# Kernel tuning notes

Measured on AMD Instinct MI355X. Metric: run time of the kernel, lower is better.

## Reference

```python
import jax, jax.numpy as jnp
import numpy as np

B, H, D = 4096, 1024, 4
SCALE = 20.0
EPS = 1e-7
LABEL_GATE = 0.01


def _layer_norm(x, g, b, eps=1e-5):
    mu = jnp.mean(x, axis=-1, keepdims=True)
    var = jnp.mean(jnp.square(x - mu), axis=-1, keepdims=True)
    return (x - mu) * jax.lax.rsqrt(var + eps) * g + b


def setup_inputs() -> dict:
    key = jax.random.key(0)
    ks = jax.random.split(key, 8)
    s = 0.02
    return {
        "pooled": jax.random.normal(ks[0], (B, H), dtype=jnp.float32),
        "labels": jax.random.uniform(ks[1], (B, D), dtype=jnp.float32),
        "ln1_g": jnp.ones((H,), jnp.float32),
        "ln1_b": jnp.zeros((H,), jnp.float32),
        "W1": jax.random.normal(ks[2], (H, H // 2), dtype=jnp.float32) * s,
        "b1": jnp.zeros((H // 2,), jnp.float32),
        "ln2_g": jnp.ones((H // 2,), jnp.float32),
        "ln2_b": jnp.zeros((H // 2,), jnp.float32),
        "W2": jax.random.normal(ks[3], (H // 2, H // 4), dtype=jnp.float32) * s,
        "b2": jnp.zeros((H // 4,), jnp.float32),
        "Wh": jax.random.normal(ks[4], (H // 4, D), dtype=jnp.float32) * s,
        "bh": jnp.zeros((D,), jnp.float32),
    }


def reference(pooled, labels, ln1_g, ln1_b, W1, b1, ln2_g, ln2_b, W2, b2, Wh, bh):
    # MLP head (dropout = identity in eval mode); exact GELU as in torch nn.GELU
    h1 = jax.nn.gelu(_layer_norm(pooled, ln1_g, ln1_b) @ W1 + b1, approximate=False)
    h2 = jax.nn.gelu(_layer_norm(h1, ln2_g, ln2_b) @ W2 + b2, approximate=False)
    logits = jax.nn.sigmoid(h2 @ Wh + bh)  # [B, D]

    # MSE term
    mse = jnp.mean(jnp.square(logits - labels))

    # Vectorized pairwise ordering loss over all i<j pairs and dims
    ldiff = labels[:, None, :] - labels[None, :, :]   # [B, B, D]
    pdiff = logits[:, None, :] - logits[None, :, :]   # [B, B, D]
    target_prob = jax.nn.sigmoid(SCALE * ldiff)
    pred_prob = jax.nn.sigmoid(SCALE * pdiff)
    bce = -target_prob * jnp.log(pred_prob + EPS) - (1.0 - target_prob) * jnp.log(1.0 - pred_prob + EPS)

    iu = jnp.triu(jnp.ones((B, B), dtype=bool), k=1)[:, :, None]  # i < j
    mask = iu & (jnp.abs(ldiff) > LABEL_GATE)
    cnt = jnp.sum(mask)
    ordering = jnp.where(cnt > 0, jnp.sum(jnp.where(mask, bce, 0.0)) / jnp.maximum(cnt, 1).astype(bce.dtype), 0.0)

    loss = 0.5 * mse + 0.5 * ordering
    return loss, logits
```

## Files before the change

### kernel.cpp

```cpp
#include <hip/hip_runtime.h>
#include <math.h>
#include <stdint.h>

typedef unsigned short u16;
typedef unsigned long long u64;
typedef __attribute__((ext_vector_type(8))) short bf16x8;
typedef __attribute__((ext_vector_type(4))) float f32x4;

#define RSQRT1_2F 0.70710678118654752440f

__device__ __forceinline__ u16 rne_bf16(float x) {
  unsigned u = __float_as_uint(x);
  return (u16)((u + 0x7FFFu + ((u >> 16) & 1u)) >> 16);
}
__device__ __forceinline__ float bf16_to_f(u16 h) {
  return __uint_as_float(((unsigned)h) << 16);
}
__device__ __forceinline__ void gload_lds16(const void* g, void* l) {
  __builtin_amdgcn_global_load_lds(
      (__attribute__((address_space(1))) void*)(uintptr_t)g,
      (__attribute__((address_space(3))) void*)(uintptr_t)l, 16, 0, 0);
}
__device__ __forceinline__ float rlane(float v, int sl) {
  return __uint_as_float((unsigned)__builtin_amdgcn_readlane((int)__float_as_uint(v), sl));
}
__device__ __forceinline__ float block_reduce_sum_f(float v, float* smem4) {
  #pragma unroll
  for (int off = 32; off > 0; off >>= 1) v += __shfl_down(v, off, 64);
  const int lane = threadIdx.x & 63;
  const int wid  = threadIdx.x >> 6;
  if (lane == 0) smem4[wid] = v;
  __syncthreads();
  float r = smem4[0] + smem4[1] + smem4[2] + smem4[3];
  __syncthreads();
  return r;
}
__device__ __forceinline__ float gelu_exact(float z) {
  return 0.5f * z * (1.0f + erff(z * RSQRT1_2F));
}

template<int H, int NPT>
__device__ __forceinline__ void ln_split_body(
    const float* __restrict__ x, const float* __restrict__ g,
    const float* __restrict__ b, u16* __restrict__ yhi, u16* __restrict__ ylo,
    int row, float* smem4) {
  const float* xr = x + (size_t)row * H;
  const int tid = threadIdx.x;
  float v[NPT];
  #pragma unroll
  for (int q = 0; q < NPT; ++q) v[q] = xr[tid + q * 256];
  float s = 0.f;
  #pragma unroll
  for (int q = 0; q < NPT; ++q) s += v[q];
  s = block_reduce_sum_f(s, smem4);
  const float mu = s * (1.0f / H);
  float s2 = 0.f;
  #pragma unroll
  for (int q = 0; q < NPT; ++q) { float d = v[q] - mu; s2 = fmaf(d, d, s2); }
  s2 = block_reduce_sum_f(s2, smem4);
  const float rstd = rsqrtf(s2 * (1.0f / H) + 1e-5f);
  #pragma unroll
  for (int q = 0; q < NPT; ++q) {
    const int c = tid + q * 256;
    const float y = (v[q] - mu) * rstd * g[c] + b[c];
    const u16 h = rne_bf16(y);
    const u16 lo = rne_bf16(y - bf16_to_f(h));
    yhi[(size_t)row * H + c] = h;
    ylo[(size_t)row * H + c] = lo;
  }
}

template<int K, int N>
__device__ __forceinline__ void wsplit_body(
    const float* __restrict__ W, u16* __restrict__ Whi, u16* __restrict__ Wlo,
    int ntile, int ktile, float* sm ) {
  const int t = threadIdx.x;
  const int n0 = ntile * 64, k0 = ktile * 64;
  #pragma unroll
  for (int q = 0; q < 16; ++q) {
    const int r = q * 4 + (t >> 6);
    sm[r * 65 + (t & 63)] = W[(size_t)(k0 + r) * N + n0 + (t & 63)];
  }
  __syncthreads();
  #pragma unroll
  for (int q = 0; q < 16; ++q) {
    const int nr = q * 4 + (t >> 6);
    const int kc = t & 63;
    const float v = sm[kc * 65 + nr];
    const u16 h = rne_bf16(v);
    const u16 lo = rne_bf16(v - bf16_to_f(h));
    Whi[(size_t)(n0 + nr) * K + k0 + kc] = h;
    Wlo[(size_t)(n0 + nr) * K + k0 + kc] = lo;
  }
}

__global__ __launch_bounds__(256) void prep_kernel(
    const float* __restrict__ pooled, const float* __restrict__ ln1_g,
    const float* __restrict__ ln1_b, const float* __restrict__ W1,
    const float* __restrict__ W2,
    u16* __restrict__ xhi, u16* __restrict__ xlo,
    u16* __restrict__ w1thi, u16* __restrict__ w1tlo,
    u16* __restrict__ w2thi, u16* __restrict__ w2tlo) {
  __shared__ float sm[64 * 65];
  const int bid = blockIdx.x;
  if (bid < 4096) {
    ln_split_body<1024, 4>(pooled, ln1_g, ln1_b, xhi, xlo, bid, sm);
  } else if (bid < 4224) {
    const int idx = bid - 4096;
    wsplit_body<1024, 512>(W1, w1thi, w1tlo, idx & 7, idx >> 3, sm);
  } else {
    const int idx = bid - 4224;
    wsplit_body<512, 256>(W2, w2thi, w2tlo, idx & 3, idx >> 2, sm);
  }
}

template<int H, int NPT>
__global__ __launch_bounds__(256) void ln_gelu_split_kernel(
    const float* __restrict__ Pa, const float* __restrict__ Pb,
    const float* __restrict__ bias, const float* __restrict__ g,
    const float* __restrict__ b, u16* __restrict__ yhi, u16* __restrict__ ylo) {
  __shared__ float smem4[4];
  const int row = blockIdx.x;
  const size_t base = (size_t)row * H;
  const int tid = threadIdx.x;
  float v[NPT];
  #pragma unroll
  for (int q = 0; q < NPT; ++q) {
    const int c = tid + q * 256;
    v[q] = gelu_exact(Pa[base + c] + Pb[base + c] + bias[c]);
  }
  float s = 0.f;
  #pragma unroll
  for (int q = 0; q < NPT; ++q) s += v[q];
  s = block_reduce_sum_f(s, smem4);
  const float mu = s * (1.0f / H);
  float s2 = 0.f;
  #pragma unroll
  for (int q = 0; q < NPT; ++q) { float d = v[q] - mu; s2 = fmaf(d, d, s2); }
  s2 = block_reduce_sum_f(s2, smem4);
  const float rstd = rsqrtf(s2 * (1.0f / H) + 1e-5f);
  #pragma unroll
  for (int q = 0; q < NPT; ++q) {
    const int c = tid + q * 256;
    const float y = (v[q] - mu) * rstd * g[c] + b[c];
    const u16 h = rne_bf16(y);
    const u16 lo = rne_bf16(y - bf16_to_f(h));
    yhi[base + c] = h;
    ylo[base + c] = lo;
  }
}

template<int M, int N, int K, int KCH>
__global__ __launch_bounds__(256, 2) void gemm_bf16x3_partial(
    const u16* __restrict__ Ahi, const u16* __restrict__ Alo,
    const u16* __restrict__ Bhi, const u16* __restrict__ Blo,
    float* __restrict__ P, double* zclr) {
  if (zclr && blockIdx.x == 0 && blockIdx.y == 0 && blockIdx.z == 0 &&
      threadIdx.x < 32) {
    zclr[threadIdx.x] = 0.0;
    zclr[32 + threadIdx.x] = 0.0;
    ((u64*)(zclr + 64))[threadIdx.x] = 0ull;
  }
  __shared__ __align__(16) char sb[49152];
  const int t = threadIdx.x;
  const int w = t >> 6;
  const int l = t & 63;
  const int lm = l & 15, lk = l >> 4;
  const int wm = w >> 1, wn = w & 1;

  const int gx = gridDim.x, gy = gridDim.y;
  const int nwg = gx * gy * gridDim.z;
  const int bid = blockIdx.x + gx * (blockIdx.y + gy * blockIdx.z);
  int swz = (bid & 7) * (nwg >> 3) + (bid >> 3);
  const int bx = swz % gx; swz /= gx;
  const int by = swz % gy;
  const int bz = swz / gy;

  const int m0 = by * 128, n0 = bx * 64;
  const int kbase = bz * KCH;
  float* __restrict__ Pz = P + (size_t)bz * M * N;

  f32x4 acc[4][2];
  #pragma unroll
  for (int m = 0; m < 4; ++m)
    #pragma unroll
    for (int n = 0; n < 2; ++n)
      #pragma unroll
      for (int r = 0; r < 4; ++r) acc[m][n][r] = 0.f;

  const int srow = t >> 3;
  const int sslot = (t & 7) * 16;

  for (int k0 = kbase; k0 < kbase + KCH; k0 += 64) {
    #pragma unroll
    for (int q = 0; q < 4; ++q) {
      const int row = q * 32 + srow;
      const int cl = sslot ^ ((row & 7) << 4);
      const size_t gb = ((size_t)(m0 + row) * K + k0) * 2 + cl;
      gload_lds16((const char*)Ahi + gb, sb + q * 4096 + w * 1024);
      gload_lds16((const char*)Alo + gb, sb + 16384 + q * 4096 + w * 1024);
    }
    #pragma unroll
    for (int q = 0; q < 2; ++q) {
      const int row = q * 32 + srow;
      const int cl = sslot ^ ((row & 7) << 4);
      const size_t gb = ((size_t)(n0 + row) * K + k0) * 2 + cl;
      gload_lds16((const char*)Bhi + gb, sb + 32768 + q * 4096 + w * 1024);
      gload_lds16((const char*)Blo + gb, sb + 40960 + q * 4096 + w * 1024);
    }
    __syncthreads();

    #pragma unroll
    for (int kk = 0; kk < 2; ++kk) {
      const int cbase = kk * 64 + lk * 16;
      bf16x8 ah[4], al[4];
      #pragma unroll
      for (int m = 0; m < 4; ++m) {
        const int row = wm * 64 + m * 16 + lm;
        const int c = cbase ^ ((row & 7) << 4);
        ah[m] = *(const bf16x8*)(sb + row * 128 + c);
        al[m] = *(const bf16x8*)(sb + 16384 + row * 128 + c);
      }
      bf16x8 bh[2], bl[2];
      #pragma unroll
      for (int n = 0; n < 2; ++n) {
        const int row = wn * 32 + n * 16 + lm;
        const int c = cbase ^ ((row & 7) << 4);
        bh[n] = *(const bf16x8*)(sb + 32768 + row * 128 + c);
        bl[n] = *(const bf16x8*)(sb + 40960 + row * 128 + c);
      }
      #pragma unroll
      for (int m = 0; m < 4; ++m)
        #pragma unroll
        for (int n = 0; n < 2; ++n) {
          acc[m][n] = __builtin_amdgcn_mfma_f32_16x16x32_bf16(ah[m], bh[n], acc[m][n], 0, 0, 0);
          acc[m][n] = __builtin_amdgcn_mfma_f32_16x16x32_bf16(ah[m], bl[n], acc[m][n], 0, 0, 0);
          acc[m][n] = __builtin_amdgcn_mfma_f32_16x16x32_bf16(al[m], bh[n], acc[m][n], 0, 0, 0);
        }
    }
    __syncthreads();
  }

  #pragma unroll
  for (int m = 0; m < 4; ++m)
    #pragma unroll
    for (int n = 0; n < 2; ++n) {
      const int col = n0 + wn * 32 + n * 16 + lm;
      #pragma unroll
      for (int r = 0; r < 4; ++r) {
        const int row = m0 + wm * 64 + m * 16 + lk * 4 + r;
        Pz[(size_t)row * N + col] = acc[m][n][r];
      }
    }
}

template<int NZ>
__global__ __launch_bounds__(256) void head_kernel(
    const float* __restrict__ P2, const float* __restrict__ b2,
    const float* __restrict__ Wh, const float* __restrict__ bh,
    const float* __restrict__ labels,
    float* __restrict__ logits_out, float* __restrict__ To,
    float* __restrict__ Eo, float* __restrict__ Lo,
    double* __restrict__ mse_slots) {
  const int lane = threadIdx.x & 63;
  const int wv   = threadIdx.x >> 6;
  const int row  = blockIdx.x * 4 + wv;
  const size_t base = (size_t)row * 256;
  constexpr size_t ZSTRIDE = (size_t)4096 * 256;
  float a0 = 0.f, a1 = 0.f, a2 = 0.f, a3 = 0.f;
  #pragma unroll
  for (int q = 0; q < 4; ++q) {
    const int k = lane + q * 64;
    float s = b2[k];
    #pragma unroll
    for (int z = 0; z < NZ; ++z) s += P2[z * ZSTRIDE + base + k];
    const float hv = gelu_exact(s);
    const float4 wv4 = *(const float4*)&Wh[k * 4];
    a0 = fmaf(hv, wv4.x, a0); a1 = fmaf(hv, wv4.y, a1);
    a2 = fmaf(hv, wv4.z, a2); a3 = fmaf(hv, wv4.w, a3);
  }
  #pragma unroll
  for (int off = 32; off > 0; off >>= 1) {
    a0 += __shfl_down(a0, off, 64);
    a1 += __shfl_down(a1, off, 64);
    a2 += __shfl_down(a2, off, 64);
    a3 += __shfl_down(a3, off, 64);
  }
  if (lane == 0) {
    const float z[4] = {a0 + bh[0], a1 + bh[1], a2 + bh[2], a3 + bh[3]};
    float msew = 0.f;
    #pragma unroll
    for (int d = 0; d < 4; ++d) {
      const float p = 1.0f / (1.0f + expf(-z[d]));
      const float lab = labels[row * 4 + d];
      logits_out[row * 4 + d] = p;
      To[row * 4 + d] = 20.0f * p;
      Eo[row * 4 + d] = expf(20.0f * p);
      Lo[row * 4 + d] = expf(20.0f * lab);
      const float df = p - lab;
      msew = fmaf(df, df, msew);
    }
    atomicAdd(&mse_slots[row & 31], (double)msew);
  }
}

#define GFUN(t) ((t) * 64 - (t) * ((t) - 1) / 2)
#define TGATE 0.0498339962f

__global__ __launch_bounds__(256) void pairwise_kernel(
    const float* __restrict__ To, const float* __restrict__ E,
    const float* __restrict__ L, double* __restrict__ slots) {
  const int lane = threadIdx.x & 63;
  const int wv   = threadIdx.x >> 6;
  const int idx  = blockIdx.x * 4 + wv;
  const int tile = idx >> 1;
  const int jbase = (idx & 1) * 32;

  int ti = (int)((129.0f - sqrtf(fmaxf(16641.0f - 8.0f * (float)tile, 0.f))) * 0.5f);
  if (ti < 0) ti = 0; if (ti > 63) ti = 63;
  while (ti > 0 && GFUN(ti) > tile) ti--;
  while (ti < 63 && GFUN(ti + 1) <= tile) ti++;
  const int tj = ti + (tile - GFUN(ti));
  const int i0 = ti * 64, j0 = tj * 64;
  const int i = i0 + lane, j = j0 + lane;

  const float4 e4 = *(const float4*)&E[(size_t)i * 4];
  const float4 t4 = *(const float4*)&To[(size_t)i * 4];
  const float4 l4 = *(const float4*)&L[(size_t)i * 4];
  const float Ei[4] = {e4.x, e4.y, e4.z, e4.w};
  const float Ti[4] = {t4.x, t4.y, t4.z, t4.w};
  const float Li[4] = {l4.x, l4.y, l4.z, l4.w};
  const float4 ej4 = *(const float4*)&E[(size_t)j * 4];
  const float4 tj4 = *(const float4*)&To[(size_t)j * 4];
  const float4 lj4 = *(const float4*)&L[(size_t)j * 4];
  const float Ejv[4] = {ej4.x, ej4.y, ej4.z, ej4.w};
  const float Tjv[4] = {tj4.x, tj4.y, tj4.z, tj4.w};
  const float Ljv[4] = {lj4.x, lj4.y, lj4.z, lj4.w};

  const bool diag = (ti == tj);
  float acc[4] = {0.f, 0.f, 0.f, 0.f};
  int cnt = 0;
  #pragma unroll 8
  for (int s = 0; s < 32; ++s) {
    const int jj = jbase + s;
    const bool jok = !diag || (jj > lane);
    #pragma unroll
    for (int d = 0; d < 4; ++d) {
      const float Ej = rlane(Ejv[d], jj);
      const float Tj = rlane(Tjv[d], jj);
      const float Lj = rlane(Ljv[d], jj);
      const float logse = __logf(Ei[d] + Ej);
      const float tt = Li[d] * __builtin_amdgcn_rcpf(Li[d] + Lj);
      const float bce = (logse - Tj) - tt * (Ti[d] - Tj);
      const bool m = jok && (fabsf(tt - 0.5f) > TGATE);
      acc[d] += m ? bce : 0.f;
      cnt += m ? 1 : 0;
    }
  }

  float tot = (acc[0] + acc[1]) + (acc[2] + acc[3]);
  #pragma unroll
  for (int off = 32; off > 0; off >>= 1) {
    tot += __shfl_down(tot, off, 64);
    cnt += __shfl_down(cnt, off, 64);
  }
  if (lane == 0) {
    const int sl = idx & 31;
    atomicAdd(&slots[32 + sl], (double)tot);
    atomicAdd((u64*)(slots + 64) + sl, (u64)cnt);
  }
}

__global__ void finalize_kernel(const double* __restrict__ slots,
                                float* __restrict__ out) {
  const int l = threadIdx.x;
  double m = (l < 32) ? slots[l] : 0.0;
  double o = (l < 32) ? slots[32 + l] : 0.0;
  double c = (l < 32) ? (double)((const u64*)(slots + 64))[l] : 0.0;
  #pragma unroll
  for (int off = 32; off > 0; off >>= 1) {
    m += __shfl_down(m, off, 64);
    o += __shfl_down(o, off, 64);
    c += __shfl_down(c, off, 64);
  }
  if (l == 0) {
    const double mse = m / (4096.0 * 4.0);
    const double ord = (c > 0.0) ? (o / c) : 0.0;
    out[0] = (float)(0.5 * mse + 0.5 * ord);
  }
}

extern "C" void kernel_launch(void* const* d_in, const int* in_sizes, int n_in,
                              void* d_out, int out_size, void* d_ws, size_t ws_size,
                              hipStream_t stream) {
  const float* pooled = (const float*)d_in[0];
  const float* labels = (const float*)d_in[1];
  const float* ln1_g  = (const float*)d_in[2];
  const float* ln1_b  = (const float*)d_in[3];
  const float* W1     = (const float*)d_in[4];
  const float* b1     = (const float*)d_in[5];
  const float* ln2_g  = (const float*)d_in[6];
  const float* ln2_b  = (const float*)d_in[7];
  const float* W2     = (const float*)d_in[8];
  const float* b2     = (const float*)d_in[9];
  const float* Wh     = (const float*)d_in[10];
  const float* bh     = (const float*)d_in[11];
  float* out = (float*)d_out;

  char* ws = (char*)d_ws;
  u16*   xhi   = (u16*)(ws + 0);
  u16*   xlo   = (u16*)(ws + 8388608);
  u16*   w1thi = (u16*)(ws + 16777216);
  u16*   w1tlo = (u16*)(ws + 17825792);
  float* P1    = (float*)(ws + 18874368);
  u16*   h1nhi = (u16*)(ws + 0);
  u16*   h1nlo = (u16*)(ws + 4194304);
  u16*   w2thi = (u16*)(ws + 8388608);
  u16*   w2tlo = (u16*)(ws + 8650752);
  float* P2    = (float*)(ws + 8912896);
  float* Eo    = (float*)(ws + 25690112);
  float* To    = (float*)(ws + 25755648);
  float* Lo    = (float*)(ws + 25821184);
  double* slots = (double*)(ws + 25886720);

  prep_kernel<<<4256, 256, 0, stream>>>(pooled, ln1_g, ln1_b, W1, W2,
                                        xhi, xlo, w1thi, w1tlo, w2thi, w2tlo);
  gemm_bf16x3_partial<4096, 512, 1024, 512><<<dim3(8, 32, 2), 256, 0, stream>>>(
      xhi, xlo, w1thi, w1tlo, P1, nullptr);
  ln_gelu_split_kernel<512, 2><<<4096, 256, 0, stream>>>(
      P1, P1 + (size_t)4096 * 512, b1, ln2_g, ln2_b, h1nhi, h1nlo);
  gemm_bf16x3_partial<4096, 256, 512, 128><<<dim3(4, 32, 4), 256, 0, stream>>>(
      h1nhi, h1nlo, w2thi, w2tlo, P2, slots);
  head_kernel<4><<<1024, 256, 0, stream>>>(
      P2, b2, Wh, bh, labels, out + 1, To, Eo, Lo, slots);
  pairwise_kernel<<<1040, 256, 0, stream>>>(To, Eo, Lo, slots);
  finalize_kernel<<<1, 64, 0, stream>>>(slots, out);
}
```

Baseline: 190.3 us.

## Fuse all stages into one persistent kernel with software grid barriers

Replaces the seven-kernel launch chain with a single persistent 512-block kernel that runs prep, both GEMMs, LN/GELU, head, pairwise loss and finalize as phases separated by a two-level atomic grid barrier. The aim is to remove kernel launch gaps and tail effects between the small stages. Row-wise LayerNorm moves to one wave per row with shuffle-only reductions, and the GEMM now uses a double-buffered BK=32 LDS pipeline. The cost is spin-wait barriers that assume all 512 blocks are co-resident, a bounded spin that could silently break, and a fixed grid that may underuse the device in some phases.

```diff
diff --git a/kernel.cpp b/kernel.cpp
--- a/kernel.cpp
+++ b/kernel.cpp
@@ -8,6 +8,8 @@
 typedef __attribute__((ext_vector_type(4))) float f32x4;
 
 #define RSQRT1_2F 0.70710678118654752440f
+#define MB 1048576UL
+#define NBLK 512
 
 __device__ __forceinline__ u16 rne_bf16(float x) {
   unsigned u = __float_as_uint(x);
@@ -24,50 +26,36 @@
 __device__ __forceinline__ float rlane(float v, int sl) {
   return __uint_as_float((unsigned)__builtin_amdgcn_readlane((int)__float_as_uint(v), sl));
 }
-__device__ __forceinline__ float block_reduce_sum_f(float v, float* smem4) {
+__device__ __forceinline__ float wave_sum(float v) {
   #pragma unroll
-  for (int off = 32; off > 0; off >>= 1) v += __shfl_down(v, off, 64);
-  const int lane = threadIdx.x & 63;
-  const int wid  = threadIdx.x >> 6;
-  if (lane == 0) smem4[wid] = v;
-  __syncthreads();
-  float r = smem4[0] + smem4[1] + smem4[2] + smem4[3];
-  __syncthreads();
-  return r;
+  for (int off = 32; off > 0; off >>= 1) v += __shfl_xor(v, off, 64);
+  return v;
 }
 __device__ __forceinline__ float gelu_exact(float z) {
   return 0.5f * z * (1.0f + erff(z * RSQRT1_2F));
 }
 
-template<int H, int NPT>
-__device__ __forceinline__ void ln_split_body(
-    const float* __restrict__ x, const float* __restrict__ g,
-    const float* __restrict__ b, u16* __restrict__ yhi, u16* __restrict__ ylo,
-    int row, float* smem4) {
-  const float* xr = x + (size_t)row * H;
-  const int tid = threadIdx.x;
-  float v[NPT];
-  #pragma unroll
-  for (int q = 0; q < NPT; ++q) v[q] = xr[tid + q * 256];
-  float s = 0.f;
-  #pragma unroll
-  for (int q = 0; q < NPT; ++q) s += v[q];
-  s = block_reduce_sum_f(s, smem4);
-  const float mu = s * (1.0f / H);
-  float s2 = 0.f;
-  #pragma unroll
-  for (int q = 0; q < NPT; ++q) { float d = v[q] - mu; s2 = fmaf(d, d, s2); }
-  s2 = block_reduce_sum_f(s2, smem4);
-  const float rstd = rsqrtf(s2 * (1.0f / H) + 1e-5f);
-  #pragma unroll
-  for (int q = 0; q < NPT; ++q) {
-    const int c = tid + q * 256;
-    const float y = (v[q] - mu) * rstd * g[c] + b[c];
-    const u16 h = rne_bf16(y);
-    const u16 lo = rne_bf16(y - bf16_to_f(h));
-    yhi[(size_t)row * H + c] = h;
-    ylo[(size_t)row * H + c] = lo;
-  }
+__device__ __forceinline__ void grid_sync(char* bar, int phase) {
+  __syncthreads();
+  if (threadIdx.x == 0) {
+    unsigned* L1   = (unsigned*)(bar + phase * 4096);
+    unsigned* L2   = (unsigned*)(bar + phase * 4096 + 2048);
+    unsigned* flag = (unsigned*)(bar + phase * 4096 + 2176);
+    __threadfence();
+    if (atomicAdd(&L1[(blockIdx.x & 31) * 16], 1u) == 15u) {
+      if (atomicAdd(L2, 1u) == 31u) {
+        __threadfence();
+        atomicExch(flag, 1u);
+      }
+    }
+    int iters = 0;
+    while (__hip_atomic_load(flag, __ATOMIC_RELAXED, __HIP_MEMORY_SCOPE_AGENT) == 0u) {
+      __builtin_amdgcn_s_sleep(2);
+      if (++iters > (1 << 22)) break;
+    }
+    __threadfence();
+  }
+  __syncthreads();
 }
 
 template<int K, int N>
@@ -92,93 +80,27 @@
     Whi[(size_t)(n0 + nr) * K + k0 + kc] = h;
     Wlo[(size_t)(n0 + nr) * K + k0 + kc] = lo;
   }
-}
-
-__global__ __launch_bounds__(256) void prep_kernel(
-    const float* __restrict__ pooled, const float* __restrict__ ln1_g,
-    const float* __restrict__ ln1_b, const float* __restrict__ W1,
-    const float* __restrict__ W2,
-    u16* __restrict__ xhi, u16* __restrict__ xlo,
-    u16* __restrict__ w1thi, u16* __restrict__ w1tlo,
-    u16* __restrict__ w2thi, u16* __restrict__ w2tlo) {
-  __shared__ float sm[64 * 65];
-  const int bid = blockIdx.x;
-  if (bid < 4096) {
-    ln_split_body<1024, 4>(pooled, ln1_g, ln1_b, xhi, xlo, bid, sm);
-  } else if (bid < 4224) {
-    const int idx = bid - 4096;
-    wsplit_body<1024, 512>(W1, w1thi, w1tlo, idx & 7, idx >> 3, sm);
-  } else {
-    const int idx = bid - 4224;
-    wsplit_body<512, 256>(W2, w2thi, w2tlo, idx & 3, idx >> 2, sm);
-  }
-}
-
-template<int H, int NPT>
-__global__ __launch_bounds__(256) void ln_gelu_split_kernel(
-    const float* __restrict__ Pa, const float* __restrict__ Pb,
-    const float* __restrict__ bias, const float* __restrict__ g,
-    const float* __restrict__ b, u16* __restrict__ yhi, u16* __restrict__ ylo) {
-  __shared__ float smem4[4];
-  const int row = blockIdx.x;
-  const size_t base = (size_t)row * H;
-  const int tid = threadIdx.x;
-  float v[NPT];
-  #pragma unroll
-  for (int q = 0; q < NPT; ++q) {
-    const int c = tid + q * 256;
-    v[q] = gelu_exact(Pa[base + c] + Pb[base + c] + bias[c]);
-  }
-  float s = 0.f;
-  #pragma unroll
-  for (int q = 0; q < NPT; ++q) s += v[q];
-  s = block_reduce_sum_f(s, smem4);
-  const float mu = s * (1.0f / H);
-  float s2 = 0.f;
-  #pragma unroll
-  for (int q = 0; q < NPT; ++q) { float d = v[q] - mu; s2 = fmaf(d, d, s2); }
-  s2 = block_reduce_sum_f(s2, smem4);
-  const float rstd = rsqrtf(s2 * (1.0f / H) + 1e-5f);
-  #pragma unroll
-  for (int q = 0; q < NPT; ++q) {
-    const int c = tid + q * 256;
-    const float y = (v[q] - mu) * rstd * g[c] + b[c];
-    const u16 h = rne_bf16(y);
-    const u16 lo = rne_bf16(y - bf16_to_f(h));
-    yhi[base + c] = h;
-    ylo[base + c] = lo;
-  }
-}
-
-template<int M, int N, int K, int KCH>
-__global__ __launch_bounds__(256, 2) void gemm_bf16x3_partial(
-    const u16* __restrict__ Ahi, const u16* __restrict__ Alo,
-    const u16* __restrict__ Bhi, const u16* __restrict__ Blo,
-    float* __restrict__ P, double* zclr) {
-  if (zclr && blockIdx.x == 0 && blockIdx.y == 0 && blockIdx.z == 0 &&
-      threadIdx.x < 32) {
-    zclr[threadIdx.x] = 0.0;
-    zclr[32 + threadIdx.x] = 0.0;
-    ((u64*)(zclr + 64))[threadIdx.x] = 0ull;
-  }
-  __shared__ __align__(16) char sb[49152];
-  const int t = threadIdx.x;
-  const int w = t >> 6;
-  const int l = t & 63;
-  const int lm = l & 15, lk = l >> 4;
+  __syncthreads();
+}
+
+template<int NX, int MY, int NZ, int K>
+__device__ void gemm_phase(const u16* __restrict__ Ahi, const u16* __restrict__ Alo,
+                           const u16* __restrict__ Bhi, const u16* __restrict__ Blo,
+                           float* __restrict__ P, char* sb) {
+  constexpr int BN = 64, M = 4096;
+  constexpr int N = BN * NX;
+  constexpr int KCH = K / NZ;
+  constexpr int NS = KCH / 32;
+  constexpr int BUF = 24576;
+  const int t = threadIdx.x, w = t >> 6, l = t & 63, lm = l & 15, lk = l >> 4;
   const int wm = w >> 1, wn = w & 1;
-
-  const int gx = gridDim.x, gy = gridDim.y;
-  const int nwg = gx * gy * gridDim.z;
-  const int bid = blockIdx.x + gx * (blockIdx.y + gy * blockIdx.z);
-  int swz = (bid & 7) * (nwg >> 3) + (bid >> 3);
-  const int bx = swz % gx; swz /= gx;
-  const int by = swz % gy;
-  const int bz = swz / gy;
-
-  const int m0 = by * 128, n0 = bx * 64;
-  const int kbase = bz * KCH;
-  float* __restrict__ Pz = P + (size_t)bz * M * N;
+  int bid = (int)blockIdx.x;
+  bid = (bid & 7) * 64 + (bid >> 3);
+  const int z = bid / (NX * MY);
+  const int rem = bid % (NX * MY);
+  const int my = rem / NX, nx = rem % NX;
+  const int m0 = my * 128, n0 = nx * BN, kbase = z * KCH;
+  float* __restrict__ Pz = P + (size_t)z * M * N;
 
   f32x4 acc[4][2];
   #pragma unroll
@@ -188,56 +110,59 @@
       #pragma unroll
       for (int r = 0; r < 4; ++r) acc[m][n][r] = 0.f;
 
-  const int srow = t >> 3;
-  const int sslot = (t & 7) * 16;
-
-  for (int k0 = kbase; k0 < kbase + KCH; k0 += 64) {
-    #pragma unroll
-    for (int q = 0; q < 4; ++q) {
-      const int row = q * 32 + srow;
-      const int cl = sslot ^ ((row & 7) << 4);
-      const size_t gb = ((size_t)(m0 + row) * K + k0) * 2 + cl;
-      gload_lds16((const char*)Ahi + gb, sb + q * 4096 + w * 1024);
-      gload_lds16((const char*)Alo + gb, sb + 16384 + q * 4096 + w * 1024);
-    }
+  const int trow = t >> 2;
+  const int tcol = (t & 3) * 16;
+
+  auto STAGE = [&](int bufsel, int k0) {
+    char* bb = sb + bufsel * BUF;
     #pragma unroll
     for (int q = 0; q < 2; ++q) {
-      const int row = q * 32 + srow;
-      const int cl = sslot ^ ((row & 7) << 4);
-      const size_t gb = ((size_t)(n0 + row) * K + k0) * 2 + cl;
-      gload_lds16((const char*)Bhi + gb, sb + 32768 + q * 4096 + w * 1024);
-      gload_lds16((const char*)Blo + gb, sb + 40960 + q * 4096 + w * 1024);
-    }
-    __syncthreads();
-
-    #pragma unroll
-    for (int kk = 0; kk < 2; ++kk) {
-      const int cbase = kk * 64 + lk * 16;
-      bf16x8 ah[4], al[4];
-      #pragma unroll
-      for (int m = 0; m < 4; ++m) {
-        const int row = wm * 64 + m * 16 + lm;
-        const int c = cbase ^ ((row & 7) << 4);
-        ah[m] = *(const bf16x8*)(sb + row * 128 + c);
-        al[m] = *(const bf16x8*)(sb + 16384 + row * 128 + c);
-      }
-      bf16x8 bh[2], bl[2];
+      const int row = q * 64 + trow;
+      const int col = tcol ^ (((row >> 1) & 3) << 4);
+      const size_t gb = ((size_t)(m0 + row) * K + k0) * 2 + col;
+      gload_lds16((const char*)Ahi + gb, bb + q * 4096 + t * 16);
+      gload_lds16((const char*)Alo + gb, bb + 8192 + q * 4096 + t * 16);
+    }
+    {
+      const int row = trow;
+      const int col = tcol ^ (((row >> 1) & 3) << 4);
+      const size_t gb = ((size_t)(n0 + row) * K + k0) * 2 + col;
+      gload_lds16((const char*)Bhi + gb, bb + 16384 + t * 16);
+      gload_lds16((const char*)Blo + gb, bb + 20480 + t * 16);
+    }
+  };
+  auto COMPUTE = [&](int bufsel) {
+    char* bb = sb + bufsel * BUF;
+    bf16x8 ah[4], al[4], bhv[2], blv[2];
+    #pragma unroll
+    for (int m = 0; m < 4; ++m) {
+      const int row = wm * 64 + m * 16 + lm;
+      const int col = (lk * 16) ^ (((row >> 1) & 3) << 4);
+      ah[m] = *(const bf16x8*)(bb + row * 64 + col);
+      al[m] = *(const bf16x8*)(bb + 8192 + row * 64 + col);
+    }
+    #pragma unroll
+    for (int n = 0; n < 2; ++n) {
+      const int row = wn * 32 + n * 16 + lm;
+      const int col = (lk * 16) ^ (((row >> 1) & 3) << 4);
+      bhv[n] = *(const bf16x8*)(bb + 16384 + row * 64 + col);
+      blv[n] = *(const bf16x8*)(bb + 20480 + row * 64 + col);
+    }
+    #pragma unroll
+    for (int m = 0; m < 4; ++m)
       #pragma unroll
       for (int n = 0; n < 2; ++n) {
-        const int row = wn * 32 + n * 16 + lm;
-        const int c = cbase ^ ((row & 7) << 4);
-        bh[n] = *(const bf16x8*)(sb + 32768 + row * 128 + c);
-        bl[n] = *(const bf16x8*)(sb + 40960 + row * 128 + c);
-      }
-      #pragma unroll
-      for (int m = 0; m < 4; ++m)
-        #pragma unroll
-        for (int n = 0; n < 2; ++n) {
-          acc[m][n] = __builtin_amdgcn_mfma_f32_16x16x32_bf16(ah[m], bh[n], acc[m][n], 0, 0, 0);
-          acc[m][n] = __builtin_amdgcn_mfma_f32_16x16x32_bf16(ah[m], bl[n], acc[m][n], 0, 0, 0);
-          acc[m][n] = __builtin_amdgcn_mfma_f32_16x16x32_bf16(al[m], bh[n], acc[m][n], 0, 0, 0);
-        }
-    }
+        acc[m][n] = __builtin_amdgcn_mfma_f32_16x16x32_bf16(ah[m], bhv[n], acc[m][n], 0, 0, 0);
+        acc[m][n] = __builtin_amdgcn_mfma_f32_16x16x32_bf16(ah[m], blv[n], acc[m][n], 0, 0, 0);
+        acc[m][n] = __builtin_amdgcn_mfma_f32_16x16x32_bf16(al[m], bhv[n], acc[m][n], 0, 0, 0);
+      }
+  };
+
+  STAGE(0, kbase);
+  __syncthreads();
+  for (int s = 0; s < NS; ++s) {
+    if (s + 1 < NS) STAGE((s + 1) & 1, kbase + (s + 1) * 32);
+    COMPUTE(s & 1);
     __syncthreads();
   }
 
@@ -254,139 +179,239 @@
     }
 }
 
-template<int NZ>
-__global__ __launch_bounds__(256) void head_kernel(
-    const float* __restrict__ P2, const float* __restrict__ b2,
-    const float* __restrict__ Wh, const float* __restrict__ bh,
-    const float* __restrict__ labels,
-    float* __restrict__ logits_out, float* __restrict__ To,
-    float* __restrict__ Eo, float* __restrict__ Lo,
-    double* __restrict__ mse_slots) {
-  const int lane = threadIdx.x & 63;
-  const int wv   = threadIdx.x >> 6;
-  const int row  = blockIdx.x * 4 + wv;
-  const size_t base = (size_t)row * 256;
-  constexpr size_t ZSTRIDE = (size_t)4096 * 256;
-  float a0 = 0.f, a1 = 0.f, a2 = 0.f, a3 = 0.f;
-  #pragma unroll
-  for (int q = 0; q < 4; ++q) {
-    const int k = lane + q * 64;
-    float s = b2[k];
-    #pragma unroll
-    for (int z = 0; z < NZ; ++z) s += P2[z * ZSTRIDE + base + k];
-    const float hv = gelu_exact(s);
-    const float4 wv4 = *(const float4*)&Wh[k * 4];
-    a0 = fmaf(hv, wv4.x, a0); a1 = fmaf(hv, wv4.y, a1);
-    a2 = fmaf(hv, wv4.z, a2); a3 = fmaf(hv, wv4.w, a3);
-  }
-  #pragma unroll
-  for (int off = 32; off > 0; off >>= 1) {
-    a0 += __shfl_down(a0, off, 64);
-    a1 += __shfl_down(a1, off, 64);
-    a2 += __shfl_down(a2, off, 64);
-    a3 += __shfl_down(a3, off, 64);
-  }
-  if (lane == 0) {
-    const float z[4] = {a0 + bh[0], a1 + bh[1], a2 + bh[2], a3 + bh[3]};
-    float msew = 0.f;
-    #pragma unroll
-    for (int d = 0; d < 4; ++d) {
-      const float p = 1.0f / (1.0f + expf(-z[d]));
-      const float lab = labels[row * 4 + d];
-      logits_out[row * 4 + d] = p;
-      To[row * 4 + d] = 20.0f * p;
-      Eo[row * 4 + d] = expf(20.0f * p);
-      Lo[row * 4 + d] = expf(20.0f * lab);
-      const float df = p - lab;
-      msew = fmaf(df, df, msew);
-    }
-    atomicAdd(&mse_slots[row & 31], (double)msew);
-  }
-}
-
 #define GFUN(t) ((t) * 64 - (t) * ((t) - 1) / 2)
 #define TGATE 0.0498339962f
 
-__global__ __launch_bounds__(256) void pairwise_kernel(
-    const float* __restrict__ To, const float* __restrict__ E,
-    const float* __restrict__ L, double* __restrict__ slots) {
-  const int lane = threadIdx.x & 63;
-  const int wv   = threadIdx.x >> 6;
-  const int idx  = blockIdx.x * 4 + wv;
-  const int tile = idx >> 1;
-  const int jbase = (idx & 1) * 32;
-
-  int ti = (int)((129.0f - sqrtf(fmaxf(16641.0f - 8.0f * (float)tile, 0.f))) * 0.5f);
-  if (ti < 0) ti = 0; if (ti > 63) ti = 63;
-  while (ti > 0 && GFUN(ti) > tile) ti--;
-  while (ti < 63 && GFUN(ti + 1) <= tile) ti++;
-  const int tj = ti + (tile - GFUN(ti));
-  const int i0 = ti * 64, j0 = tj * 64;
-  const int i = i0 + lane, j = j0 + lane;
-
-  const float4 e4 = *(const float4*)&E[(size_t)i * 4];
-  const float4 t4 = *(const float4*)&To[(size_t)i * 4];
-  const float4 l4 = *(const float4*)&L[(size_t)i * 4];
-  const float Ei[4] = {e4.x, e4.y, e4.z, e4.w};
-  const float Ti[4] = {t4.x, t4.y, t4.z, t4.w};
-  const float Li[4] = {l4.x, l4.y, l4.z, l4.w};
-  const float4 ej4 = *(const float4*)&E[(size_t)j * 4];
-  const float4 tj4 = *(const float4*)&To[(size_t)j * 4];
-  const float4 lj4 = *(const float4*)&L[(size_t)j * 4];
-  const float Ejv[4] = {ej4.x, ej4.y, ej4.z, ej4.w};
-  const float Tjv[4] = {tj4.x, tj4.y, tj4.z, tj4.w};
-  const float Ljv[4] = {lj4.x, lj4.y, lj4.z, lj4.w};
-
-  const bool diag = (ti == tj);
-  float acc[4] = {0.f, 0.f, 0.f, 0.f};
-  int cnt = 0;
-  #pragma unroll 8
-  for (int s = 0; s < 32; ++s) {
-    const int jj = jbase + s;
-    const bool jok = !diag || (jj > lane);
-    #pragma unroll
-    for (int d = 0; d < 4; ++d) {
-      const float Ej = rlane(Ejv[d], jj);
-      const float Tj = rlane(Tjv[d], jj);
-      const float Lj = rlane(Ljv[d], jj);
-      const float logse = __logf(Ei[d] + Ej);
-      const float tt = Li[d] * __builtin_amdgcn_rcpf(Li[d] + Lj);
-      const float bce = (logse - Tj) - tt * (Ti[d] - Tj);
-      const bool m = jok && (fabsf(tt - 0.5f) > TGATE);
-      acc[d] += m ? bce : 0.f;
-      cnt += m ? 1 : 0;
-    }
-  }
-
-  float tot = (acc[0] + acc[1]) + (acc[2] + acc[3]);
-  #pragma unroll
-  for (int off = 32; off > 0; off >>= 1) {
-    tot += __shfl_down(tot, off, 64);
-    cnt += __shfl_down(cnt, off, 64);
-  }
-  if (lane == 0) {
-    const int sl = idx & 31;
-    atomicAdd(&slots[32 + sl], (double)tot);
-    atomicAdd((u64*)(slots + 64) + sl, (u64)cnt);
-  }
-}
-
-__global__ void finalize_kernel(const double* __restrict__ slots,
-                                float* __restrict__ out) {
-  const int l = threadIdx.x;
-  double m = (l < 32) ? slots[l] : 0.0;
-  double o = (l < 32) ? slots[32 + l] : 0.0;
-  double c = (l < 32) ? (double)((const u64*)(slots + 64))[l] : 0.0;
-  #pragma unroll
-  for (int off = 32; off > 0; off >>= 1) {
-    m += __shfl_down(m, off, 64);
-    o += __shfl_down(o, off, 64);
-    c += __shfl_down(c, off, 64);
-  }
-  if (l == 0) {
-    const double mse = m / (4096.0 * 4.0);
-    const double ord = (c > 0.0) ? (o / c) : 0.0;
-    out[0] = (float)(0.5 * mse + 0.5 * ord);
+__global__ __launch_bounds__(256, 2) void mega_kernel(
+    const float* __restrict__ pooled, const float* __restrict__ labels,
+    const float* __restrict__ ln1_g, const float* __restrict__ ln1_b,
+    const float* __restrict__ W1, const float* __restrict__ b1,
+    const float* __restrict__ ln2_g, const float* __restrict__ ln2_b,
+    const float* __restrict__ W2, const float* __restrict__ b2,
+    const float* __restrict__ Wh, const float* __restrict__ bh,
+    float* __restrict__ out, char* __restrict__ ws) {
+  __shared__ __align__(16) char sb[49152];
+
+  u16*   xhi   = (u16*)(ws);
+  u16*   xlo   = (u16*)(ws + 8 * MB);
+  u16*   w1thi = (u16*)(ws + 16 * MB);
+  u16*   w1tlo = (u16*)(ws + 17 * MB);
+  u16*   w2thi = (u16*)(ws + 18 * MB);
+  u16*   w2tlo = (u16*)(ws + 18 * MB + 262144);
+  float* P1    = (float*)(ws + 19 * MB);
+  u16*   h1nhi = (u16*)(ws + 35 * MB);
+  u16*   h1nlo = (u16*)(ws + 39 * MB);
+  float* P2    = (float*)(ws + 43 * MB);
+  float* Eo    = (float*)(ws + 59 * MB);
+  float* To    = (float*)(ws + 59 * MB + 65536);
+  float* Lo    = (float*)(ws + 59 * MB + 131072);
+  char*  bar   = ws + 60 * MB;
+  double* S    = (double*)(ws + 60 * MB + 24576);
+
+  const int t = threadIdx.x, w = t >> 6, l = t & 63;
+  const int bid = (int)blockIdx.x;
+  const int gw = bid * 4 + w;
+
+  {
+    #pragma unroll
+    for (int pass = 0; pass < 2; ++pass) {
+      const int row = gw + pass * 2048;
+      const float* xr = pooled + (size_t)row * 1024;
+      float v[16];
+      #pragma unroll
+      for (int q = 0; q < 16; ++q) v[q] = xr[l + q * 64];
+      float s = 0.f;
+      #pragma unroll
+      for (int q = 0; q < 16; ++q) s += v[q];
+      s = wave_sum(s);
+      const float mu = s * (1.0f / 1024.0f);
+      float s2 = 0.f;
+      #pragma unroll
+      for (int q = 0; q < 16; ++q) { float d = v[q] - mu; s2 = fmaf(d, d, s2); }
+      s2 = wave_sum(s2);
+      const float rstd = rsqrtf(s2 * (1.0f / 1024.0f) + 1e-5f);
+      const size_t base = (size_t)row * 1024;
+      #pragma unroll
+      for (int q = 0; q < 16; ++q) {
+        const int c = l + q * 64;
+        const float y = (v[q] - mu) * rstd * ln1_g[c] + ln1_b[c];
+        const u16 h = rne_bf16(y);
+        xhi[base + c] = h;
+        xlo[base + c] = rne_bf16(y - bf16_to_f(h));
+      }
+    }
+    if (bid < 160) {
+      __syncthreads();
+      float* sm = (float*)sb;
+      if (bid < 128) wsplit_body<1024, 512>(W1, w1thi, w1tlo, bid & 7, bid >> 3, sm);
+      else           wsplit_body<512, 256>(W2, w2thi, w2tlo, (bid - 128) & 3, (bid - 128) >> 2, sm);
+    }
+  }
+  grid_sync(bar, 0);
+
+  gemm_phase<8, 32, 2, 1024>(xhi, xlo, w1thi, w1tlo, P1, sb);
+  grid_sync(bar, 1);
+
+  {
+    constexpr size_t ZS1 = (size_t)4096 * 512;
+    #pragma unroll
+    for (int pass = 0; pass < 2; ++pass) {
+      const int row = gw + pass * 2048;
+      const size_t base = (size_t)row * 512;
+      float v[8];
+      #pragma unroll
+      for (int q = 0; q < 8; ++q) {
+        const int c = l + q * 64;
+        float s = b1[c] + P1[base + c] + P1[ZS1 + base + c];
+        v[q] = gelu_exact(s);
+      }
+      float s = 0.f;
+      #pragma unroll
+      for (int q = 0; q < 8; ++q) s += v[q];
+      s = wave_sum(s);
+      const float mu = s * (1.0f / 512.0f);
+      float s2 = 0.f;
+      #pragma unroll
+      for (int q = 0; q < 8; ++q) { float d = v[q] - mu; s2 = fmaf(d, d, s2); }
+      s2 = wave_sum(s2);
+      const float rstd = rsqrtf(s2 * (1.0f / 512.0f) + 1e-5f);
+      #pragma unroll
+      for (int q = 0; q < 8; ++q) {
+        const int c = l + q * 64;
+        const float y = (v[q] - mu) * rstd * ln2_g[c] + ln2_b[c];
+        const u16 h = rne_bf16(y);
+        h1nhi[base + c] = h;
+        h1nlo[base + c] = rne_bf16(y - bf16_to_f(h));
+      }
+    }
+  }
+  grid_sync(bar, 2);
+
+  gemm_phase<4, 32, 4, 512>(h1nhi, h1nlo, w2thi, w2tlo, P2, sb);
+  grid_sync(bar, 3);
+
+  {
+    constexpr size_t ZS2 = (size_t)4096 * 256;
+    #pragma unroll
+    for (int pass = 0; pass < 2; ++pass) {
+      const int row = gw + pass * 2048;
+      const size_t base = (size_t)row * 256;
+      float a0 = 0.f, a1 = 0.f, a2 = 0.f, a3 = 0.f;
+      #pragma unroll
+      for (int q = 0; q < 4; ++q) {
+        const int k = l + q * 64;
+        float s = b2[k];
+        #pragma unroll
+        for (int z = 0; z < 4; ++z) s += P2[z * ZS2 + base + k];
+        const float hv = gelu_exact(s);
+        const float4 w4 = *(const float4*)&Wh[k * 4];
+        a0 = fmaf(hv, w4.x, a0); a1 = fmaf(hv, w4.y, a1);
+        a2 = fmaf(hv, w4.z, a2); a3 = fmaf(hv, w4.w, a3);
+      }
+      #pragma unroll
+      for (int off = 32; off > 0; off >>= 1) {
+        a0 += __shfl_down(a0, off, 64);
+        a1 += __shfl_down(a1, off, 64);
+        a2 += __shfl_down(a2, off, 64);
+        a3 += __shfl_down(a3, off, 64);
+      }
+      if (l == 0) {
+        const float z[4] = {a0 + bh[0], a1 + bh[1], a2 + bh[2], a3 + bh[3]};
+        float msew = 0.f;
+        #pragma unroll
+        for (int d = 0; d < 4; ++d) {
+          const float p = 1.0f / (1.0f + expf(-z[d]));
+          const float lab = labels[row * 4 + d];
+          out[1 + row * 4 + d] = p;
+          To[row * 4 + d] = 20.0f * p;
+          Eo[row * 4 + d] = expf(20.0f * p);
+          Lo[row * 4 + d] = expf(20.0f * lab);
+          const float df = p - lab;
+          msew = fmaf(df, df, msew);
+        }
+        atomicAdd(&S[row & 255], (double)msew);
+      }
+    }
+  }
+  grid_sync(bar, 4);
+
+  {
+    double* ordS = S + 256;
+    u64*    cntS = (u64*)(S + 320);
+    auto PAIR = [&](int u) {
+      const int tile = u >> 1;
+      const int jbase = (u & 1) * 32;
+      int ti = (int)((129.0f - sqrtf(fmaxf(16641.0f - 8.0f * (float)tile, 0.f))) * 0.5f);
+      if (ti < 0) ti = 0; if (ti > 63) ti = 63;
+      while (ti > 0 && GFUN(ti) > tile) ti--;
+      while (ti < 63 && GFUN(ti + 1) <= tile) ti++;
+      const int tj = ti + (tile - GFUN(ti));
+      const int i = ti * 64 + l, j = tj * 64 + l;
+      const float4 e4 = *(const float4*)&Eo[(size_t)i * 4];
+      const float4 t4 = *(const float4*)&To[(size_t)i * 4];
+      const float4 l4 = *(const float4*)&Lo[(size_t)i * 4];
+      const float Ei[4] = {e4.x, e4.y, e4.z, e4.w};
+      const float Ti[4] = {t4.x, t4.y, t4.z, t4.w};
+      const float Li[4] = {l4.x, l4.y, l4.z, l4.w};
+      const float4 ej4 = *(const float4*)&Eo[(size_t)j * 4];
+      const float4 tj4 = *(const float4*)&To[(size_t)j * 4];
+      const float4 lj4 = *(const float4*)&Lo[(size_t)j * 4];
+      const float Ejv[4] = {ej4.x, ej4.y, ej4.z, ej4.w};
+      const float Tjv[4] = {tj4.x, tj4.y, tj4.z, tj4.w};
+      const float Ljv[4] = {lj4.x, lj4.y, lj4.z, lj4.w};
+      const bool diag = (ti == tj);
+      float acc[4] = {0.f, 0.f, 0.f, 0.f};
+      int cnt = 0;
+      #pragma unroll 8
+      for (int s = 0; s < 32; ++s) {
+        const int jj = jbase + s;
+        const bool jok = !diag || (jj > l);
+        #pragma unroll
+        for (int d = 0; d < 4; ++d) {
+          const float Ej = rlane(Ejv[d], jj);
+          const float Tj = rlane(Tjv[d], jj);
+          const float Lj = rlane(Ljv[d], jj);
+          const float logse = __logf(Ei[d] + Ej);
+          const float tt = Li[d] * __builtin_amdgcn_rcpf(Li[d] + Lj);
+          const float bce = (logse - Tj) - tt * (Ti[d] - Tj);
+          const bool m = jok && (fabsf(tt - 0.5f) > TGATE);
+          acc[d] += m ? bce : 0.f;
+          cnt += m ? 1 : 0;
+        }
+      }
+      float tot = (acc[0] + acc[1]) + (acc[2] + acc[3]);
+      #pragma unroll
+      for (int off = 32; off > 0; off >>= 1) {
+        tot += __shfl_down(tot, off, 64);
+        cnt += __shfl_down(cnt, off, 64);
+      }
+      if (l == 0) {
+        const int sl = u & 63;
+        atomicAdd(&ordS[sl], (double)tot);
+        atomicAdd(&cntS[sl], (u64)cnt);
+      }
+    };
+    PAIR(gw);
+    PAIR(gw + 2048);
+    if (gw < 64) PAIR(gw + 4096);
+  }
+  grid_sync(bar, 5);
+
+  if (bid == 0 && w == 0) {
+    double m = S[l] + S[l + 64] + S[l + 128] + S[l + 192];
+    double o = S[256 + l];
+    double c = (double)((u64*)(S + 320))[l];
+    #pragma unroll
+    for (int off = 32; off > 0; off >>= 1) {
+      m += __shfl_down(m, off, 64);
+      o += __shfl_down(o, off, 64);
+      c += __shfl_down(c, off, 64);
+    }
+    if (l == 0) {
+      const double mse = m / (4096.0 * 4.0);
+      const double ord = (c > 0.0) ? (o / c) : 0.0;
+      out[0] = (float)(0.5 * mse + 0.5 * ord);
+    }
   }
 }
 
@@ -406,33 +431,9 @@
   const float* Wh     = (const float*)d_in[10];
   const float* bh     = (const float*)d_in[11];
   float* out = (float*)d_out;
-
-  char* ws = (char*)d_ws;
-  u16*   xhi   = (u16*)(ws + 0);
-  u16*   xlo   = (u16*)(ws + 8388608);
-  u16*   w1thi = (u16*)(ws + 16777216);
-  u16*   w1tlo = (u16*)(ws + 17825792);
-  float* P1    = (float*)(ws + 18874368);
-  u16*   h1nhi = (u16*)(ws + 0);
-  u16*   h1nlo = (u16*)(ws + 4194304);
-  u16*   w2thi = (u16*)(ws + 8388608);
-  u16*   w2tlo = (u16*)(ws + 8650752);
-  float* P2    = (float*)(ws + 8912896);
-  float* Eo    = (float*)(ws + 25690112);
-  float* To    = (float*)(ws + 25755648);
-  float* Lo    = (float*)(ws + 25821184);
-  double* slots = (double*)(ws + 25886720);
-
-  prep_kernel<<<4256, 256, 0, stream>>>(pooled, ln1_g, ln1_b, W1, W2,
-                                        xhi, xlo, w1thi, w1tlo, w2thi, w2tlo);
-  gemm_bf16x3_partial<4096, 512, 1024, 512><<<dim3(8, 32, 2), 256, 0, stream>>>(
-      xhi, xlo, w1thi, w1tlo, P1, nullptr);
-  ln_gelu_split_kernel<512, 2><<<4096, 256, 0, stream>>>(
-      P1, P1 + (size_t)4096 * 512, b1, ln2_g, ln2_b, h1nhi, h1nlo);
-  gemm_bf16x3_partial<4096, 256, 512, 128><<<dim3(4, 32, 4), 256, 0, stream>>>(
-      h1nhi, h1nlo, w2thi, w2tlo, P2, slots);
-  head_kernel<4><<<1024, 256, 0, stream>>>(
-      P2, b2, Wh, bh, labels, out + 1, To, Eo, Lo, slots);
-  pairwise_kernel<<<1040, 256, 0, stream>>>(To, Eo, Lo, slots);
-  finalize_kernel<<<1, 64, 0, stream>>>(slots, out);
-}
+  char*  ws  = (char*)d_ws;
+
+  hipMemsetAsync(ws + 60 * MB, 0, 32768, stream);
+  mega_kernel<<<NBLK, 256, 0, stream>>>(pooled, labels, ln1_g, ln1_b, W1, b1,
+                                        ln2_g, ln2_b, W2, b2, Wh, bh, out, ws);
+}
```

After: 293.9 us. 54.4% more time.
